# Performance work log

Measured on AMD Instinct MI355X. Metric: run time of the kernel, lower is better.

The kernel has to match this reference:

```python
import jax, jax.numpy as jnp
import numpy as np

B, S, D = 2, 2048, 1024
H, HK, HD = 16, 4, 64          # query heads, kv heads, head dim = D//H
WIN = 1024                     # sliding attention window
E, K, DH = 8, 2, 2048          # experts, top_k, expert hidden (== d_head ctor arg)
ATTN_EPS, FFN_EPS = 1e-5, 1e-6
ROPE_THETA = 10000.0


def setup_inputs() -> dict:
    key = jax.random.key(0)
    ks = jax.random.split(key, 9)
    sc = 0.02
    # real rotary frequencies for positions [start_pos, start_pos+S)
    start_pos = 0
    inv_freq = 1.0 / (ROPE_THETA ** (jnp.arange(0, HD, 2, dtype=jnp.float32) / HD))  # [HD//2]
    pos = jnp.arange(start_pos, start_pos + S, dtype=jnp.float32)
    ang = pos[:, None] * inv_freq[None, :]  # [S, HD//2]
    return {
        'x': jax.random.normal(ks[0], (B, S, D), jnp.float32),
        'freqs_cos': jnp.cos(ang),
        'freqs_sin': jnp.sin(ang),
        'attn_norm_w': jnp.ones((D,), jnp.float32),
        'wq': jax.random.normal(ks[1], (D, H * HD), jnp.float32) * sc,
        'wk': jax.random.normal(ks[2], (D, HK * HD), jnp.float32) * sc,
        'wv': jax.random.normal(ks[3], (D, HK * HD), jnp.float32) * sc,
        'wo': jax.random.normal(ks[4], (H * HD, D), jnp.float32) * sc,
        'ffn_norm_w': jnp.ones((D,), jnp.float32),
        'router_w': jax.random.normal(ks[5], (D, E), jnp.float32) * sc,
        'w1': jax.random.normal(ks[6], (E, D, DH), jnp.float32) * sc,
        'w2': jax.random.normal(ks[7], (E, DH, D), jnp.float32) * sc,
        'start_pos': start_pos,
    }


def _rmsnorm(x, w, eps):
    return x * jax.lax.rsqrt(jnp.mean(x * x, axis=-1, keepdims=True) + eps) * w


def _rope(t, cos, sin):
    # t: [B,S,N,HD]; cos/sin: [S,HD//2] -> complex rotation on consecutive pairs
    shp = t.shape
    t = t.reshape(shp[:-1] + (HD // 2, 2))
    t0, t1 = t[..., 0], t[..., 1]
    c = cos[None, :, None, :]
    s = sin[None, :, None, :]
    r = jnp.stack([t0 * c - t1 * s, t0 * s + t1 * c], axis=-1)
    return r.reshape(shp)


def reference(x, freqs_cos, freqs_sin, attn_norm_w, wq, wk, wv, wo,
              ffn_norm_w, router_w, w1, w2, start_pos):
    # ---- attention sublayer (RMSNorm -> GQA sliding-window attn) ----
    hn = _rmsnorm(x, attn_norm_w, ATTN_EPS)
    q = (hn @ wq).reshape(B, S, H, HD)
    k = (hn @ wk).reshape(B, S, HK, HD)
    v = (hn @ wv).reshape(B, S, HK, HD)
    q = _rope(q, freqs_cos, freqs_sin)
    k = _rope(k, freqs_cos, freqs_sin)
    rep = H // HK
    k = jnp.repeat(k, rep, axis=2)  # [B,S,H,HD]
    v = jnp.repeat(v, rep, axis=2)
    scale = 1.0 / np.sqrt(HD).astype(np.float32)
    scores = jnp.einsum('bqhd,bkhd->bhqk', q, k) * scale  # [B,H,S,S]
    qi = jnp.arange(S) + start_pos
    kj = jnp.arange(S) + start_pos
    mask = (kj[None, :] <= qi[:, None]) & (qi[:, None] - kj[None, :] < WIN)
    scores = jnp.where(mask[None, None], scores, jnp.float32(-1e30))
    attn = jax.nn.softmax(scores, axis=-1)
    o = jnp.einsum('bhqk,bkhd->bqhd', attn, v).reshape(B, S, H * HD)
    h = x + o @ wo

    # ---- MoE sublayer (RMSNorm -> router top-k -> expert FFNs) ----
    fn = _rmsnorm(h, ffn_norm_w, FFN_EPS).reshape(-1, D)  # [T,D], T=B*S
    probs = jax.nn.softmax(fn @ router_w, axis=-1)        # [T,E]
    top_vals, top_idx = jax.lax.top_k(probs, K)           # [T,K]
    gates = top_vals / jnp.sum(top_vals, axis=-1, keepdims=True)
    gmat = jnp.sum(jax.nn.one_hot(top_idx, E, dtype=fn.dtype) * gates[..., None], axis=1)  # [T,E]
    moe = jnp.zeros_like(fn)
    for e in range(E):  # fixed small expert count
        moe = moe + gmat[:, e:e + 1] * (jax.nn.silu(fn @ w1[e]) @ w2[e])
    return h + moe.reshape(B, S, D)
```

## Files before the change

kernel.cpp:

```cpp
#include <hip/hip_runtime.h>
#include <hip/hip_bf16.h>

using bf16 = __hip_bfloat16;
typedef __attribute__((ext_vector_type(8))) short bf16x8;
typedef __attribute__((ext_vector_type(4))) short short4v;
typedef __attribute__((ext_vector_type(4))) float f32x4;

#define DEV static __device__ __forceinline__

DEV float b2f(bf16 v) { return __bfloat162float(v); }
DEV bf16  f2b(float f) { return __float2bfloat16(f); }
DEV short bbits(float f) { bf16 h = __float2bfloat16(f); short u; __builtin_memcpy(&u, &h, 2); return u; }
DEV float sb2f(short s) {
  unsigned u = ((unsigned)(unsigned short)s) << 16;
  float f; __builtin_memcpy(&f, &u, 4); return f;
}

#define GL2LDS(g, l)                                                        \
  __builtin_amdgcn_global_load_lds(                                         \
      (const __attribute__((address_space(1))) void*)(g),                   \
      (__attribute__((address_space(3))) void*)(l), 16, 0, 0)

__global__ __launch_bounds__(256) void transpose_convert(
    const float* __restrict__ src, bf16* __restrict__ dst, int K, int N) {
  __shared__ float tile[64][65];
  int n0 = blockIdx.x * 64, k0 = blockIdx.y * 64;
  src += (size_t)blockIdx.z * K * N;
  dst += (size_t)blockIdx.z * K * N;
  int t = threadIdx.x;
  int rr = t >> 4, cc = (t & 15) * 4;
#pragma unroll
  for (int p = 0; p < 4; ++p) {
    int r = rr + p * 16;
    const float4 v = *(const float4*)&src[(size_t)(k0 + r) * N + n0 + cc];
    tile[r][cc] = v.x; tile[r][cc + 1] = v.y; tile[r][cc + 2] = v.z; tile[r][cc + 3] = v.w;
  }
  __syncthreads();
#pragma unroll
  for (int p = 0; p < 4; ++p) {
    int nr = rr + p * 16;
    short4v o;
    o[0] = bbits(tile[cc + 0][nr]);
    o[1] = bbits(tile[cc + 1][nr]);
    o[2] = bbits(tile[cc + 2][nr]);
    o[3] = bbits(tile[cc + 3][nr]);
    *(short4v*)&dst[(size_t)(n0 + nr) * K + k0 + cc] = o;
  }
}

__global__ __launch_bounds__(256) void rmsnorm_kernel(
    const float* __restrict__ x, const float* __restrict__ w,
    bf16* __restrict__ o, float eps) {
  int row = blockIdx.x;
  const float* xr = x + (size_t)row * 1024;
  int t = threadIdx.x;
  float4 v = *(const float4*)&xr[t * 4];
  float ss = v.x * v.x + v.y * v.y + v.z * v.z + v.w * v.w;
#pragma unroll
  for (int d = 32; d; d >>= 1) ss += __shfl_down(ss, d);
  __shared__ float red[4];
  if ((t & 63) == 0) red[t >> 6] = ss;
  __syncthreads();
  float sum = red[0] + red[1] + red[2] + red[3];
  float sc = rsqrtf(sum * (1.f / 1024.f) + eps);
  const float4 wv = *(const float4*)&w[t * 4];
  short4v pk;
  pk[0] = bbits(v.x * sc * wv.x);
  pk[1] = bbits(v.y * sc * wv.y);
  pk[2] = bbits(v.z * sc * wv.z);
  pk[3] = bbits(v.w * sc * wv.w);
  *(short4v*)&o[(size_t)row * 1024 + t * 4] = pk;
}

__global__ __launch_bounds__(256) void rmsnorm_router(
    const float* __restrict__ h, const float* __restrict__ w,
    const float* __restrict__ rw, bf16* __restrict__ fn,
    float* __restrict__ gates, int* __restrict__ eidx) {
  int row = blockIdx.x;
  const float* hr = h + (size_t)row * 1024;
  int t = threadIdx.x;
  float4 v = *(const float4*)&hr[t * 4];
  float ss = v.x * v.x + v.y * v.y + v.z * v.z + v.w * v.w;
#pragma unroll
  for (int d = 32; d; d >>= 1) ss += __shfl_down(ss, d);
  __shared__ float red[4];
  __shared__ float red2[4][8];
  if ((t & 63) == 0) red[t >> 6] = ss;
  __syncthreads();
  float sum = red[0] + red[1] + red[2] + red[3];
  float sc = rsqrtf(sum * (1.f / 1024.f) + 1e-6f);
  const float4 wv = *(const float4*)&w[t * 4];
  float f0 = v.x * sc * wv.x, f1 = v.y * sc * wv.y;
  float f2 = v.z * sc * wv.z, f3 = v.w * sc * wv.w;
  short4v pk;
  pk[0] = bbits(f0); pk[1] = bbits(f1); pk[2] = bbits(f2); pk[3] = bbits(f3);
  *(short4v*)&fn[(size_t)row * 1024 + t * 4] = pk;
  const float* rr = rw + (size_t)t * 4 * 8;
  float lg[8];
#pragma unroll
  for (int e = 0; e < 8; ++e)
    lg[e] = f0 * rr[e] + f1 * rr[8 + e] + f2 * rr[16 + e] + f3 * rr[24 + e];
#pragma unroll
  for (int d = 32; d; d >>= 1)
#pragma unroll
    for (int e = 0; e < 8; ++e) lg[e] += __shfl_down(lg[e], d);
  if ((t & 63) == 0)
#pragma unroll
    for (int e = 0; e < 8; ++e) red2[t >> 6][e] = lg[e];
  __syncthreads();
  if (t == 0) {
    float L[8];
#pragma unroll
    for (int e = 0; e < 8; ++e)
      L[e] = red2[0][e] + red2[1][e] + red2[2][e] + red2[3][e];
    int e0 = 0; float v0 = L[0];
#pragma unroll
    for (int e = 1; e < 8; ++e) if (L[e] > v0) { v0 = L[e]; e0 = e; }
    int e1 = -1; float v1 = -1e30f;
#pragma unroll
    for (int e = 0; e < 8; ++e) if (e != e0 && L[e] > v1) { v1 = L[e]; e1 = e; }
    float r1 = expf(v1 - v0);
    float den = 1.f + r1;
    gates[row * 2] = 1.f / den;
    gates[row * 2 + 1] = r1 / den;
    eidx[row * 2] = e0;
    eidx[row * 2 + 1] = e1;
  }
}

template <int MODE>
__global__ __launch_bounds__(256) void gemm_bt(
    const bf16* __restrict__ A, const bf16* __restrict__ Bt,
    int M, int N, int Kd,
    bf16* __restrict__ outb, bf16* __restrict__ outk, bf16* __restrict__ outv,
    float* __restrict__ outf, const float* __restrict__ resid,
    const float* __restrict__ fcos, const float* __restrict__ fsin,
    const int* __restrict__ counts, const int* __restrict__ offsets,
    const int* __restrict__ tok, const float* __restrict__ gatel) {
  int count = M, off = 0;
  const bf16* Ap = A;
  const bf16* Bp = Bt;
  int mb, nb;
  if (MODE == 2 || MODE == 3) {
    int e = blockIdx.y;
    count = counts[e]; off = offsets[e];
    Bp = Bt + (size_t)e * Kd * N;
    if (MODE == 3) Ap = A + (size_t)off * Kd;
    mb = blockIdx.z * 128; nb = blockIdx.x * 128;
  } else {
    int gx = gridDim.x;
    int flat = blockIdx.y * gx + blockIdx.x;
    int cpx = (gx * gridDim.y) >> 3;
    int swz = (flat & 7) * cpx + (flat >> 3);
    mb = (swz / gx) * 128; nb = (swz % gx) * 128;
  }
  if (mb >= count) return;

  __shared__ __align__(16) bf16 As[2][128 * 32];
  __shared__ __align__(16) bf16 Bs[2][128 * 32];

  int t = threadIdx.x;
  int lane = t & 63, wid = t >> 6;

  const bf16* agl[2];
  const bf16* bgl[2];
#pragma unroll
  for (int iss = 0; iss < 2; ++iss) {
    int p = iss * 256 + wid * 64 + lane;
    int row = p >> 2, cs = p & 3;
    int c = cs ^ (row & 3);
    int m = mb + row;
    const bf16* abase;
    if (MODE == 2) {
      int tokid = (m < count) ? tok[off + m] : 0;
      abase = A + (size_t)tokid * Kd;
    } else {
      int mm = (m < count) ? m : 0;
      abase = Ap + (size_t)mm * Kd;
    }
    agl[iss] = abase + c * 8;
    bgl[iss] = Bp + (size_t)(nb + row) * Kd + c * 8;
  }

  int wr = (wid >> 1) * 64, wc = (wid & 1) * 64;
  int lr = lane & 15, lkc = lane >> 4;

  auto stage = [&](int buf, int kt) {
#pragma unroll
    for (int iss = 0; iss < 2; ++iss) {
      GL2LDS(agl[iss] + kt * 32, &As[buf][(iss * 256 + wid * 64) * 8]);
      GL2LDS(bgl[iss] + kt * 32, &Bs[buf][(iss * 256 + wid * 64) * 8]);
    }
  };

  const f32x4 fzero = {0.f, 0.f, 0.f, 0.f};
  f32x4 acc[4][4];
#pragma unroll
  for (int i = 0; i < 4; ++i)
#pragma unroll
    for (int j = 0; j < 4; ++j) acc[i][j] = fzero;

  int nk = Kd >> 5;
  stage(0, 0);
  __syncthreads();
  for (int kt = 0; kt < nk; ++kt) {
    int cur = kt & 1;
    if (kt + 1 < nk) stage(cur ^ 1, kt + 1);
    bf16x8 af[4], bfr[4];
#pragma unroll
    for (int i = 0; i < 4; ++i) {
      int r = wr + i * 16 + lr;
      af[i] = *(const bf16x8*)&As[cur][r * 32 + ((lkc ^ (r & 3)) * 8)];
    }
#pragma unroll
    for (int j = 0; j < 4; ++j) {
      int r = wc + j * 16 + lr;
      bfr[j] = *(const bf16x8*)&Bs[cur][r * 32 + ((lkc ^ (r & 3)) * 8)];
    }
#pragma unroll
    for (int i = 0; i < 4; ++i)
#pragma unroll
      for (int j = 0; j < 4; ++j)
        acc[i][j] = __builtin_amdgcn_mfma_f32_16x16x32_bf16(af[i], bfr[j], acc[i][j], 0, 0, 0);
    __syncthreads();
  }

  int rq = lane >> 4;
#pragma unroll
  for (int i = 0; i < 4; ++i) {
#pragma unroll
    for (int j = 0; j < 4; ++j) {
      if (MODE == 5) {
        int n = nb + wc + j * 16 + lr;
        if (n >= 1280) {
          int vcol = n - 1280;
          int kh = vcol >> 6, d = vcol & 63;
          int m0 = mb + wr + i * 16 + rq * 4;
          int bb = m0 >> 11, s = m0 & 2047;
          short4v pk;
#pragma unroll
          for (int r = 0; r < 4; ++r) pk[r] = bbits(acc[i][j][r]);
          *(short4v*)&outv[((size_t)((bb * 4 + kh) * 64 + d)) * 2048 + s] = pk;
        } else {
          int ii = (n & 63) >> 1;
          bool odd = n & 1;
#pragma unroll
          for (int r = 0; r < 4; ++r) {
            int m = mb + wr + i * 16 + rq * 4 + r;
            int s = m & 2047;
            float v = acc[i][j][r];
            float vp = __shfl_xor(v, 1);
            float c = fcos[s * 32 + ii], sn = fsin[s * 32 + ii];
            float o = odd ? (vp * sn + v * c) : (v * c - vp * sn);
            if (n < 1024) outb[(size_t)m * 1024 + n] = f2b(o);
            else          outk[(size_t)m * 256 + (n - 1024)] = f2b(o);
          }
        }
      } else {
#pragma unroll
        for (int r = 0; r < 4; ++r) {
          int m = mb + wr + i * 16 + rq * 4 + r;
          int n = nb + wc + j * 16 + lr;
          float v = acc[i][j][r];
          if (MODE == 1) {
            outf[(size_t)m * N + n] = resid[(size_t)m * N + n] + v;
          } else if (MODE == 2) {
            if (m < count) {
              float sg = 1.f / (1.f + expf(-v));
              outb[(size_t)(off + m) * N + n] = f2b(v * sg);
            }
          } else if (MODE == 3) {
            if (m < count) {
              int row = off + m;
              outb[(size_t)row * N + n] = f2b(gatel[row] * v);
            }
          }
        }
      }
    }
  }
}

__global__ __launch_bounds__(256) void attn_kernel(
    const bf16* __restrict__ q, const bf16* __restrict__ kb,
    const bf16* __restrict__ vt, bf16* __restrict__ o) {
  int qb = blockIdx.x, h = blockIdx.y, b = blockIdx.z;
  int kh = h >> 2;
  int t = threadIdx.x;
  int lane = t & 63, wid = t >> 6;
  int lr = lane & 15, lkc = lane >> 4;
  int q0 = qb * 64;
  int qrow = q0 + wid * 16;

  __shared__ __align__(16) bf16 Ks[64 * 64];
  __shared__ __align__(16) bf16 Vs[64 * 64];
  __shared__ __align__(16) bf16 Ps[4][16 * 72];

  bf16x8 aq[2];
#pragma unroll
  for (int kk = 0; kk < 2; ++kk)
    aq[kk] = *(const bf16x8*)&q[(size_t)(b * 2048 + qrow + lr) * 1024 + h * 64 + kk * 32 + lkc * 8];

  const f32x4 fzero = {0.f, 0.f, 0.f, 0.f};
  f32x4 oacc[4];
  float mrun[4], lrun[4];
#pragma unroll
  for (int r = 0; r < 4; ++r) { oacc[r] = fzero; mrun[r] = -1e30f; lrun[r] = 0.f; }

  int klo = q0 - 1023; if (klo < 0) klo = 0;
  int tlo = klo >> 6, thi = q0 >> 6;
  int skey = t >> 3;
  int sch = t & 7;

  for (int kt = tlo; kt <= thi; ++kt) {
    int kbase = kt * 64;
#pragma unroll
    for (int pp = 0; pp < 2; ++pp) {
      int key = skey + pp * 32;
      bf16x8 kv = *(const bf16x8*)&kb[(size_t)(b * 2048 + kbase + key) * 256 + kh * 64 + sch * 8];
      *(bf16x8*)&Ks[key * 64 + ((sch ^ (key & 7)) * 8)] = kv;
      bf16x8 vv = *(const bf16x8*)&vt[((size_t)((b * 4 + kh) * 64 + key)) * 2048 + kbase + sch * 8];
      *(bf16x8*)&Vs[key * 64 + ((sch ^ (key & 7)) * 8)] = vv;
    }
    __syncthreads();

    f32x4 sacc[4];
#pragma unroll
    for (int nt = 0; nt < 4; ++nt) sacc[nt] = fzero;
#pragma unroll
    for (int nt = 0; nt < 4; ++nt)
#pragma unroll
      for (int kk = 0; kk < 2; ++kk) {
        int r = nt * 16 + lr;
        bf16x8 bk = *(const bf16x8*)&Ks[r * 64 + (((kk * 4 + lkc) ^ (r & 7)) * 8)];
        sacc[nt] = __builtin_amdgcn_mfma_f32_16x16x32_bf16(aq[kk], bk, sacc[nt], 0, 0, 0);
      }

    float sval[4][4], mt[4];
    int qg = qrow + lkc * 4;
#pragma unroll
    for (int r = 0; r < 4; ++r) mt[r] = -1e30f;
#pragma unroll
    for (int nt = 0; nt < 4; ++nt) {
      int kkey = kbase + nt * 16 + lr;
#pragma unroll
      for (int r = 0; r < 4; ++r) {
        float s = sacc[nt][r] * 0.125f;
        int qq = qg + r;
        bool valid = (kkey <= qq) && (qq - kkey < 1024);
        s = valid ? s : -1e30f;
        sval[nt][r] = s;
        mt[r] = fmaxf(mt[r], s);
      }
    }
#pragma unroll
    for (int d = 1; d < 16; d <<= 1)
#pragma unroll
      for (int r = 0; r < 4; ++r) mt[r] = fmaxf(mt[r], __shfl_xor(mt[r], d));
    float alpha[4], rs[4];
#pragma unroll
    for (int r = 0; r < 4; ++r) {
      float mn = fmaxf(mrun[r], mt[r]);
      alpha[r] = __expf(mrun[r] - mn);
      mrun[r] = mn;
      rs[r] = 0.f;
    }
#pragma unroll
    for (int nt = 0; nt < 4; ++nt)
#pragma unroll
      for (int r = 0; r < 4; ++r) {
        float pv = __expf(sval[nt][r] - mrun[r]);
        sval[nt][r] = pv;
        rs[r] += pv;
      }
#pragma unroll
    for (int d = 1; d < 16; d <<= 1)
#pragma unroll
      for (int r = 0; r < 4; ++r) rs[r] += __shfl_xor(rs[r], d);
#pragma unroll
    for (int r = 0; r < 4; ++r) lrun[r] = lrun[r] * alpha[r] + rs[r];
#pragma unroll
    for (int dt = 0; dt < 4; ++dt) {
      f32x4 t4 = oacc[dt];
#pragma unroll
      for (int r = 0; r < 4; ++r) t4[r] *= alpha[r];
      oacc[dt] = t4;
    }

    bf16* pw = &Ps[wid][0];
#pragma unroll
    for (int nt = 0; nt < 4; ++nt)
#pragma unroll
      for (int r = 0; r < 4; ++r)
        pw[(lkc * 4 + r) * 72 + nt * 16 + lr] = f2b(sval[nt][r]);
    __syncthreads();

    bf16x8 pa[2];
#pragma unroll
    for (int kk2 = 0; kk2 < 2; ++kk2)
      pa[kk2] = *(const bf16x8*)&pw[lr * 72 + kk2 * 32 + lkc * 8];
#pragma unroll
    for (int dt = 0; dt < 4; ++dt)
#pragma unroll
      for (int kk2 = 0; kk2 < 2; ++kk2) {
        int rrow = dt * 16 + lr;
        bf16x8 bv = *(const bf16x8*)&Vs[rrow * 64 + (((kk2 * 4 + lkc) ^ (rrow & 7)) * 8)];
        oacc[dt] = __builtin_amdgcn_mfma_f32_16x16x32_bf16(pa[kk2], bv, oacc[dt], 0, 0, 0);
      }
    __syncthreads();
  }

#pragma unroll
  for (int dt = 0; dt < 4; ++dt)
#pragma unroll
    for (int r = 0; r < 4; ++r) {
      int qq = qrow + lkc * 4 + r;
      int dd = dt * 16 + lr;
      o[(size_t)(b * 2048 + qq) * 1024 + h * 64 + dd] = f2b(oacc[dt][r] / lrun[r]);
    }
}

__global__ __launch_bounds__(1024) void moe_setup(
    const int* __restrict__ eidx, const float* __restrict__ gates,
    int* __restrict__ counts, int* __restrict__ offsets,
    int* __restrict__ tok, float* __restrict__ gatel, int* __restrict__ inv) {
  __shared__ int hist[8];
  __shared__ int cur[8];
  int t = threadIdx.x;
  if (t < 8) hist[t] = 0;
  __syncthreads();
  int e[8];
#pragma unroll
  for (int c = 0; c < 8; ++c) {
    e[c] = eidx[c * 1024 + t];
    atomicAdd(&hist[e[c]], 1);
  }
  __syncthreads();
  if (t == 0) {
    int o = 0;
#pragma unroll
    for (int i = 0; i < 8; ++i) {
      offsets[i] = o; cur[i] = o;
      int cnt = hist[i]; counts[i] = cnt; o += cnt;
    }
  }
  __syncthreads();
#pragma unroll
  for (int c = 0; c < 8; ++c) {
    int i = c * 1024 + t;
    int pos = atomicAdd(&cur[e[c]], 1);
    tok[pos] = i >> 1;
    gatel[pos] = gates[i];
    inv[i] = pos;
  }
}

__global__ __launch_bounds__(256) void final_add(
    const float* __restrict__ h, const bf16* __restrict__ y2,
    const int* __restrict__ inv, float* __restrict__ out) {
  int tokid = blockIdx.x;
  int t = threadIdx.x;
  int i0 = inv[tokid * 2], i1 = inv[tokid * 2 + 1];
  size_t base = (size_t)tokid * 1024 + t * 4;
  float4 a = *(const float4*)&h[base];
  short4v p0 = *(const short4v*)&y2[(size_t)i0 * 1024 + t * 4];
  short4v p1 = *(const short4v*)&y2[(size_t)i1 * 1024 + t * 4];
  float4 o;
  o.x = a.x + sb2f(p0[0]) + sb2f(p1[0]);
  o.y = a.y + sb2f(p0[1]) + sb2f(p1[1]);
  o.z = a.z + sb2f(p0[2]) + sb2f(p1[2]);
  o.w = a.w + sb2f(p0[3]) + sb2f(p1[3]);
  *(float4*)&out[base] = o;
}

extern "C" void kernel_launch(void* const* d_in, const int* in_sizes, int n_in,
                              void* d_out, int out_size, void* d_ws, size_t ws_size,
                              hipStream_t stream) {
  const float* x    = (const float*)d_in[0];
  const float* fcos = (const float*)d_in[1];
  const float* fsin = (const float*)d_in[2];
  const float* attw = (const float*)d_in[3];
  const float* wq   = (const float*)d_in[4];
  const float* wk   = (const float*)d_in[5];
  const float* wv   = (const float*)d_in[6];
  const float* wo   = (const float*)d_in[7];
  const float* ffnw = (const float*)d_in[8];
  const float* rw   = (const float*)d_in[9];
  const float* w1   = (const float*)d_in[10];
  const float* w2   = (const float*)d_in[11];
  float* out = (float*)d_out;

  const int M = 4096;
  char* p = (char*)d_ws;
  auto alloc = [&](size_t b) { char* r = p; p += (b + 255) & ~(size_t)255; return r; };

  bf16* hn     = (bf16*)alloc((size_t)M * 1024 * 2);
  bf16* qb     = (bf16*)alloc((size_t)M * 1024 * 2);
  bf16* kbuf   = (bf16*)alloc((size_t)M * 256 * 2);
  bf16* vt     = (bf16*)alloc((size_t)M * 256 * 2);
  bf16* ob     = (bf16*)alloc((size_t)M * 1024 * 2);
  float* hbuf  = (float*)alloc((size_t)M * 1024 * 4);
  bf16* fn     = (bf16*)alloc((size_t)M * 1024 * 2);
  bf16* wqkvt  = (bf16*)alloc((size_t)1536 * 1024 * 2);
  bf16* wot    = (bf16*)alloc((size_t)1024 * 1024 * 2);
  bf16* w1t    = (bf16*)alloc((size_t)8 * 2048 * 1024 * 2);
  bf16* w2t    = (bf16*)alloc((size_t)8 * 1024 * 2048 * 2);
  bf16* act    = (bf16*)alloc((size_t)8192 * 2048 * 2);
  bf16* y2     = (bf16*)alloc((size_t)8192 * 1024 * 2);
  float* gates = (float*)alloc((size_t)M * 2 * 4);
  int* eidx    = (int*)alloc((size_t)M * 2 * 4);
  int* counts  = (int*)alloc(8 * 4);
  int* offsets = (int*)alloc(8 * 4);
  int* tok     = (int*)alloc(8192 * 4);
  int* inv     = (int*)alloc(8192 * 4);
  float* gatel = (float*)alloc(8192 * 4);

  transpose_convert<<<dim3(16, 16, 1), 256, 0, stream>>>(wq, wqkvt, 1024, 1024);
  transpose_convert<<<dim3(4, 16, 1), 256, 0, stream>>>(wk, wqkvt + (size_t)1024 * 1024, 1024, 256);
  transpose_convert<<<dim3(4, 16, 1), 256, 0, stream>>>(wv, wqkvt + (size_t)1280 * 1024, 1024, 256);
  transpose_convert<<<dim3(16, 16, 1), 256, 0, stream>>>(wo, wot, 1024, 1024);
  transpose_convert<<<dim3(32, 16, 8), 256, 0, stream>>>(w1, w1t, 1024, 2048);
  transpose_convert<<<dim3(16, 32, 8), 256, 0, stream>>>(w2, w2t, 2048, 1024);

  rmsnorm_kernel<<<M, 256, 0, stream>>>(x, attw, hn, 1e-5f);

  gemm_bt<5><<<dim3(12, 32, 1), 256, 0, stream>>>(hn, wqkvt, M, 1536, 1024,
      qb, kbuf, vt, nullptr, nullptr, fcos, fsin, nullptr, nullptr, nullptr, nullptr);

  attn_kernel<<<dim3(32, 16, 2), 256, 0, stream>>>(qb, kbuf, vt, ob);

  gemm_bt<1><<<dim3(8, 32, 1), 256, 0, stream>>>(ob, wot, M, 1024, 1024,
      nullptr, nullptr, nullptr, hbuf, x, nullptr, nullptr, nullptr, nullptr, nullptr, nullptr);

  rmsnorm_router<<<M, 256, 0, stream>>>(hbuf, ffnw, rw, fn, gates, eidx);
  moe_setup<<<1, 1024, 0, stream>>>(eidx, gates, counts, offsets, tok, gatel, inv);

  gemm_bt<2><<<dim3(16, 8, 16), 256, 0, stream>>>(fn, w1t, M, 2048, 1024,
      act, nullptr, nullptr, nullptr, nullptr, nullptr, nullptr, counts, offsets, tok, nullptr);
  gemm_bt<3><<<dim3(8, 8, 16), 256, 0, stream>>>(act, w2t, M, 1024, 2048,
      y2, nullptr, nullptr, nullptr, nullptr, nullptr, nullptr, counts, offsets, tok, gatel);

  final_add<<<M, 256, 0, stream>>>(hbuf, y2, inv, out);
}
```

Baseline: 354.8 us.

## Add dedicated 256x256-tile 8-wave MoE up-projection GEMM with interleaved staging

Replaces the generic 128x128 gathered-token expert GEMM for the first MoE projection with a specialized 512-thread kernel using 256x256 tiles, 64-wide K steps, and four interleaved phases that overlap global-to-LDS loads with MFMA work, using setprio and barriers. Larger tiles raise data reuse per loaded byte and cut the block count. The cost is heavy register and LDS use (one block per CU) and more wasted work on partially filled expert tiles, since 256-row tiles are coarser than per-expert token counts. The generic kernel drops its MODE 2 path and clamps padded rows to the last valid row.

```diff
diff --git a/kernel.cpp b/kernel.cpp
--- a/kernel.cpp
+++ b/kernel.cpp
@@ -128,6 +128,179 @@
   }
 }
 
+__global__ __launch_bounds__(512, 1) void gemm_moe1_8p(
+    const bf16* __restrict__ A, const bf16* __restrict__ Bt,
+    bf16* __restrict__ outb,
+    const int* __restrict__ counts, const int* __restrict__ offsets,
+    const int* __restrict__ tok) {
+  constexpr int KD = 1024, NN = 2048, NK = 16;
+  int e = blockIdx.y;
+  int count = counts[e], off = offsets[e];
+  int mb = blockIdx.z * 256, nb = blockIdx.x * 256;
+  if (mb >= count) return;
+  const bf16* Bp = Bt + (size_t)e * KD * NN;
+
+  __shared__ __align__(16) bf16 As[2][256 * 64];
+  __shared__ __align__(16) bf16 Bs[2][256 * 64];
+
+  int t = threadIdx.x;
+  int lane = t & 63, wid = t >> 6;
+  int wm = wid >> 2, wn = wid & 3;
+  int lr = lane & 15, lkc = lane >> 4;
+  int swz = lr & 7;
+
+  const bf16* aglb[2][2];
+  const bf16* bglb[2][2];
+#pragma unroll
+  for (int h = 0; h < 2; ++h)
+#pragma unroll
+    for (int l = 0; l < 2; ++l) {
+      int c = l * 512 + t;
+      int row = h * 128 + (c >> 3);
+      int kc = (c & 7) ^ (row & 7);
+      int m = mb + row;
+      int mm = (m < count) ? m : (count - 1);
+      aglb[h][l] = A + (size_t)tok[off + mm] * KD + kc * 8;
+      bglb[h][l] = Bp + (size_t)(nb + row) * KD + kc * 8;
+    }
+
+#define STG_A(buf, h, kt)                                                    \
+  do {                                                                       \
+    GL2LDS(aglb[h][0] + (kt) * 64, &As[buf][((h) * 1024 + t) * 8]);          \
+    GL2LDS(aglb[h][1] + (kt) * 64, &As[buf][((h) * 1024 + 512 + t) * 8]);    \
+  } while (0)
+#define STG_B(buf, h, kt)                                                    \
+  do {                                                                       \
+    GL2LDS(bglb[h][0] + (kt) * 64, &Bs[buf][((h) * 1024 + t) * 8]);          \
+    GL2LDS(bglb[h][1] + (kt) * 64, &Bs[buf][((h) * 1024 + 512 + t) * 8]);    \
+  } while (0)
+
+  const f32x4 fzero = {0.f, 0.f, 0.f, 0.f};
+  f32x4 acc[8][4];
+#pragma unroll
+  for (int i = 0; i < 8; ++i)
+#pragma unroll
+    for (int j = 0; j < 4; ++j) acc[i][j] = fzero;
+
+  STG_A(0, 0, 0); STG_A(0, 1, 0);
+  STG_B(0, 0, 0); STG_B(0, 1, 0);
+  STG_A(1, 0, 1); STG_A(1, 1, 1);
+  asm volatile("s_waitcnt vmcnt(4)" ::: "memory");
+  __builtin_amdgcn_s_barrier();
+
+  for (int kt = 0; kt < NK; ++kt) {
+    int cur = kt & 1;
+    bf16x8 af[8][2];
+#pragma unroll
+    for (int i = 0; i < 8; ++i)
+#pragma unroll
+      for (int kk = 0; kk < 2; ++kk)
+        af[i][kk] = *(const bf16x8*)&As[cur][(wm * 128 + i * 16 + lr) * 64 +
+                                            (((kk * 4 + lkc) ^ swz) * 8)];
+    bf16x8 b0[2];
+#pragma unroll
+    for (int kk = 0; kk < 2; ++kk)
+      b0[kk] = *(const bf16x8*)&Bs[cur][(wn * 64 + 0 * 16 + lr) * 64 +
+                                        (((kk * 4 + lkc) ^ swz) * 8)];
+    if (kt + 1 < NK) STG_B(cur ^ 1, 0, kt + 1);
+    asm volatile("" ::: "memory");
+    __builtin_amdgcn_s_barrier();
+    __builtin_amdgcn_sched_barrier(0);
+    __builtin_amdgcn_s_setprio(1);
+#pragma unroll
+    for (int i = 0; i < 8; ++i)
+#pragma unroll
+      for (int kk = 0; kk < 2; ++kk)
+        acc[i][0] = __builtin_amdgcn_mfma_f32_16x16x32_bf16(af[i][kk], b0[kk], acc[i][0], 0, 0, 0);
+    __builtin_amdgcn_s_setprio(0);
+    __builtin_amdgcn_sched_barrier(0);
+    asm volatile("" ::: "memory");
+    __builtin_amdgcn_s_barrier();
+    bf16x8 b1[2];
+#pragma unroll
+    for (int kk = 0; kk < 2; ++kk)
+      b1[kk] = *(const bf16x8*)&Bs[cur][(wn * 64 + 1 * 16 + lr) * 64 +
+                                        (((kk * 4 + lkc) ^ swz) * 8)];
+    if (kt + 1 < NK) STG_B(cur ^ 1, 1, kt + 1);
+    asm volatile("" ::: "memory");
+    __builtin_amdgcn_s_barrier();
+    __builtin_amdgcn_sched_barrier(0);
+    __builtin_amdgcn_s_setprio(1);
+#pragma unroll
+    for (int i = 0; i < 8; ++i)
+#pragma unroll
+      for (int kk = 0; kk < 2; ++kk)
+        acc[i][1] = __builtin_amdgcn_mfma_f32_16x16x32_bf16(af[i][kk], b1[kk], acc[i][1], 0, 0, 0);
+    __builtin_amdgcn_s_setprio(0);
+    __builtin_amdgcn_sched_barrier(0);
+    asm volatile("" ::: "memory");
+    __builtin_amdgcn_s_barrier();
+    bf16x8 b2[2];
+#pragma unroll
+    for (int kk = 0; kk < 2; ++kk)
+      b2[kk] = *(const bf16x8*)&Bs[cur][(wn * 64 + 2 * 16 + lr) * 64 +
+                                        (((kk * 4 + lkc) ^ swz) * 8)];
+    if (kt + 2 < NK) STG_A(cur, 0, kt + 2);
+    asm volatile("" ::: "memory");
+    __builtin_amdgcn_s_barrier();
+    __builtin_amdgcn_sched_barrier(0);
+    __builtin_amdgcn_s_setprio(1);
+#pragma unroll
+    for (int i = 0; i < 8; ++i)
+#pragma unroll
+      for (int kk = 0; kk < 2; ++kk)
+        acc[i][2] = __builtin_amdgcn_mfma_f32_16x16x32_bf16(af[i][kk], b2[kk], acc[i][2], 0, 0, 0);
+    __builtin_amdgcn_s_setprio(0);
+    __builtin_amdgcn_sched_barrier(0);
+    asm volatile("" ::: "memory");
+    __builtin_amdgcn_s_barrier();
+    bf16x8 b3[2];
+#pragma unroll
+    for (int kk = 0; kk < 2; ++kk)
+      b3[kk] = *(const bf16x8*)&Bs[cur][(wn * 64 + 3 * 16 + lr) * 64 +
+                                        (((kk * 4 + lkc) ^ swz) * 8)];
+    if (kt + 2 < NK) STG_A(cur, 1, kt + 2);
+    asm volatile("" ::: "memory");
+    __builtin_amdgcn_s_barrier();
+    __builtin_amdgcn_sched_barrier(0);
+    __builtin_amdgcn_s_setprio(1);
+#pragma unroll
+    for (int i = 0; i < 8; ++i)
+#pragma unroll
+      for (int kk = 0; kk < 2; ++kk)
+        acc[i][3] = __builtin_amdgcn_mfma_f32_16x16x32_bf16(af[i][kk], b3[kk], acc[i][3], 0, 0, 0);
+    __builtin_amdgcn_s_setprio(0);
+    __builtin_amdgcn_sched_barrier(0);
+    if (kt == NK - 2) {
+      asm volatile("s_waitcnt vmcnt(0)" ::: "memory");
+    } else if (kt < NK - 2) {
+      asm volatile("s_waitcnt vmcnt(4)" ::: "memory");
+    }
+    asm volatile("" ::: "memory");
+    __builtin_amdgcn_s_barrier();
+  }
+#undef STG_A
+#undef STG_B
+
+  int rq = lane >> 4;
+#pragma unroll
+  for (int i = 0; i < 8; ++i) {
+#pragma unroll
+    for (int j = 0; j < 4; ++j) {
+#pragma unroll
+      for (int r = 0; r < 4; ++r) {
+        int m = mb + wm * 128 + i * 16 + rq * 4 + r;
+        if (m < count) {
+          int n = nb + wn * 64 + j * 16 + lr;
+          float v = acc[i][j][r];
+          float sg = 1.f / (1.f + expf(-v));
+          outb[(size_t)(off + m) * 2048 + n] = f2b(v * sg);
+        }
+      }
+    }
+  }
+}
+
 template <int MODE>
 __global__ __launch_bounds__(256) void gemm_bt(
     const bf16* __restrict__ A, const bf16* __restrict__ Bt,
@@ -141,11 +314,11 @@
   const bf16* Ap = A;
   const bf16* Bp = Bt;
   int mb, nb;
-  if (MODE == 2 || MODE == 3) {
+  if (MODE == 3) {
     int e = blockIdx.y;
     count = counts[e]; off = offsets[e];
     Bp = Bt + (size_t)e * Kd * N;
-    if (MODE == 3) Ap = A + (size_t)off * Kd;
+    Ap = A + (size_t)off * Kd;
     mb = blockIdx.z * 128; nb = blockIdx.x * 128;
   } else {
     int gx = gridDim.x;
@@ -170,14 +343,8 @@
     int row = p >> 2, cs = p & 3;
     int c = cs ^ (row & 3);
     int m = mb + row;
-    const bf16* abase;
-    if (MODE == 2) {
-      int tokid = (m < count) ? tok[off + m] : 0;
-      abase = A + (size_t)tokid * Kd;
-    } else {
-      int mm = (m < count) ? m : 0;
-      abase = Ap + (size_t)mm * Kd;
-    }
+    int mm = (m < count) ? m : (count > 0 ? count - 1 : 0);
+    const bf16* abase = Ap + (size_t)((MODE == 3) ? mm : m) * Kd;
     agl[iss] = abase + c * 8;
     bgl[iss] = Bp + (size_t)(nb + row) * Kd + c * 8;
   }
@@ -264,11 +431,6 @@
           float v = acc[i][j][r];
           if (MODE == 1) {
             outf[(size_t)m * N + n] = resid[(size_t)m * N + n] + v;
-          } else if (MODE == 2) {
-            if (m < count) {
-              float sg = 1.f / (1.f + expf(-v));
-              outb[(size_t)(off + m) * N + n] = f2b(v * sg);
-            }
           } else if (MODE == 3) {
             if (m < count) {
               int row = off + m;
@@ -535,8 +697,7 @@
   rmsnorm_router<<<M, 256, 0, stream>>>(hbuf, ffnw, rw, fn, gates, eidx);
   moe_setup<<<1, 1024, 0, stream>>>(eidx, gates, counts, offsets, tok, gatel, inv);
 
-  gemm_bt<2><<<dim3(16, 8, 16), 256, 0, stream>>>(fn, w1t, M, 2048, 1024,
-      act, nullptr, nullptr, nullptr, nullptr, nullptr, nullptr, counts, offsets, tok, nullptr);
+  gemm_moe1_8p<<<dim3(8, 8, 8), 512, 0, stream>>>(fn, w1t, act, counts, offsets, tok);
   gemm_bt<3><<<dim3(8, 8, 16), 256, 0, stream>>>(act, w2t, M, 1024, 2048,
       y2, nullptr, nullptr, nullptr, nullptr, nullptr, nullptr, counts, offsets, tok, gatel);
 
```

Result: slower. 423.0 us (+19.2%).
